# Performance work log

Measured on AMD Instinct MI355X. Metric: run time of the kernel, lower is better.

## Reference

```python
import jax, jax.numpy as jnp
import numpy as np

B, C, H, W = 16, 1, 2048, 128
K8 = 8  # conv1/conv2 expand in_dim -> in_dim*8 channels


def setup_inputs() -> dict:
    key = jax.random.key(0)
    k = jax.random.split(key, 6)
    x = jax.random.normal(k[0], (B, C, H, W), dtype=jnp.float32)
    # 1x1 convs with in_channels=1 reduce to per-output-channel scale + bias
    w1 = jax.random.normal(k[1], (K8,), dtype=jnp.float32) * 0.5
    b1 = jax.random.normal(k[2], (K8,), dtype=jnp.float32) * 0.1
    w2 = jax.random.normal(k[3], (K8,), dtype=jnp.float32) * 0.5
    b2 = jax.random.normal(k[4], (K8,), dtype=jnp.float32) * 0.1
    gamma = jax.random.normal(k[5], (1,), dtype=jnp.float32) * 0.1
    return {"x": x, "w1": w1, "b1": b1, "w2": w2, "b2": b2, "gamma": gamma}


def reference(x, w1, b1, w2, b2, gamma):
    # x: (B,1,H,W)
    # conv1 / conv2: 1x1 conv, 1 -> 8 channels == scale+bias broadcast
    p1 = x * w1[None, :, None, None] + b1[None, :, None, None]  # (B,8,H,W)
    p2 = x * w2[None, :, None, None] + b2[None, :, None, None]  # (B,8,H,W)
    # proj_query: permute(0,2,1,3).reshape(B,H,8W)
    q = p1.transpose(0, 2, 1, 3).reshape(B, H, K8 * W)
    # proj_key: permute(0,1,3,2).reshape(B,8W,H)
    k_ = p2.transpose(0, 1, 3, 2).reshape(B, K8 * W, H)
    energy = jnp.einsum('bhd,bdg->bhg', q, k_)  # (B,H,H)
    mn = energy.min(axis=2, keepdims=True)
    mx = energy.max(axis=2, keepdims=True)
    energy = (energy - mn) / (mx - mn + 1e-8)
    attn = jax.nn.softmax(energy, axis=2)  # (B,H,H)
    # attention.reshape(B,1,H,H) @ x (B,1,H,W) -> (B,1,H,W)
    out = jnp.einsum('bhg,bgw->bhw', attn, x[:, 0])[:, None]
    return gamma * out + x
```

## Files before the change

kernel.cpp:

```cpp
#include <hip/hip_runtime.h>
#include <hip/hip_bf16.h>

#define B_ 16
#define H_ 2048
#define W_ 128

using f32x4  = __attribute__((ext_vector_type(4))) float;
using bf16x8 = __attribute__((ext_vector_type(8))) short;

#define GLOAD_LDS16(g, l) __builtin_amdgcn_global_load_lds( \
    (const __attribute__((address_space(1))) unsigned int*)(g), \
    (__attribute__((address_space(3))) unsigned int*)(l), 16, 0, 0)

__device__ inline short bf16bits(float f) {
    union { __hip_bfloat16 h; short s; } u;
    u.h = __float2bfloat16(f);
    return u.s;
}

__global__ __launch_bounds__(512) void prep(const float* __restrict__ x,
                                            const float* __restrict__ b1,
                                            const float* __restrict__ w2,
                                            short* __restrict__ Xbt,
                                            short* __restrict__ XTt,
                                            float* __restrict__ cs) {
    __shared__ short xs2[8192];
    int b  = blockIdx.x >> 5;
    int g0 = (blockIdx.x & 31) * 64;
    const float* xb = x + ((size_t)b * H_ + g0) * W_;
    short* outb = Xbt + (size_t)b * H_ * W_ + (size_t)g0 * W_;
    short* outt = XTt + (size_t)b * H_ * W_ + (size_t)g0 * W_;
    int t = threadIdx.x;
    float Cc = 0.f;
#pragma unroll
    for (int c = 0; c < 8; ++c) Cc += b1[c] * w2[c];

#pragma unroll
    for (int half = 0; half < 2; ++half) {
        int p = half * 512 + t;
        int row = p >> 4, seg = p & 15;
        const float* src = xb + (size_t)row * W_ + seg * 8;
        float4 v0 = *reinterpret_cast<const float4*>(src);
        float4 v1 = *reinterpret_cast<const float4*>(src + 4);
        bf16x8 v;
        v[0] = bf16bits(v0.x); v[1] = bf16bits(v0.y);
        v[2] = bf16bits(v0.z); v[3] = bf16bits(v0.w);
        v[4] = bf16bits(v1.x); v[5] = bf16bits(v1.y);
        v[6] = bf16bits(v1.z); v[7] = bf16bits(v1.w);
        int chunk = ((row >> 4) * 4 + (seg >> 2)) * 64 + (seg & 3) * 16 + (row & 15);
        *reinterpret_cast<bf16x8*>(outb + (size_t)chunk * 8) = v;
        float s = (v0.x + v0.y + v0.z + v0.w) + (v1.x + v1.y + v1.z + v1.w);
        s += __shfl_xor(s, 1); s += __shfl_xor(s, 2);
        s += __shfl_xor(s, 4); s += __shfl_xor(s, 8);
        if (seg == 0) cs[b * H_ + g0 + row] = Cc * s;
        int c8 = seg ^ ((row >> 3) & 3);
        *reinterpret_cast<bf16x8*>(&xs2[row * 128 + c8 * 8]) = v;
    }
    __syncthreads();
    {
        int r2 = t & 7, qp = (t >> 3) & 3, nt2 = (t >> 5) & 7, kt = t >> 8;
        int w0 = nt2 * 16 + r2 * 2;
        int c8p = (w0 >> 3) ^ qp;
        int gb = kt * 32 + qp * 8;
        bf16x8 lo, hi;
#pragma unroll
        for (int jj = 0; jj < 8; ++jj) {
            unsigned u = *reinterpret_cast<const unsigned*>(
                &xs2[(gb + jj) * 128 + c8p * 8 + (w0 & 7)]);
            lo[jj] = (short)(u & 0xffffu);
            hi[jj] = (short)(u >> 16);
        }
        *reinterpret_cast<bf16x8*>(outt + (size_t)(t * 2) * 8) = lo;
        *reinterpret_cast<bf16x8*>(outt + (size_t)(t * 2 + 1) * 8) = hi;
    }
}

__global__ __launch_bounds__(512, 4) void fused_attn(
    const float* __restrict__ x,
    const short* __restrict__ Xbt, const short* __restrict__ XTt,
    const float* __restrict__ cs,
    const float* __restrict__ w1, const float* __restrict__ w2,
    const float* __restrict__ gamma, float* __restrict__ out) {
    __shared__ __align__(16) char stgA[2][8192];
    __shared__ __align__(16) char stgV[2][8192];
    __shared__ __align__(16) char pb[2][4096];
    __shared__ float red_mn[4][2][16];
    __shared__ float red_mx[4][2][16];
    __shared__ float zred[4][2][16];

    float A = 0.f;
#pragma unroll
    for (int c = 0; c < 8; ++c) A += w1[c] * w2[c];

    int tid = threadIdx.x;
    int wv = tid >> 6, lane = tid & 63;
    int wh = wv >> 1, wg = wv & 1;
    int q = lane >> 4, r = lane & 15;

    int bid = blockIdx.x;
    int swz = (bid & 7) * 64 + (bid >> 3);
    int b = swz >> 5, hb = swz & 31;
    int h_base = hb * 64;

    const char* xbt = (const char*)(Xbt + (size_t)b * H_ * W_);
    const char* xtt = (const char*)(XTt + (size_t)b * H_ * W_);
    const float* csb = cs + b * H_;

    bf16x8 afr[4];
#pragma unroll
    for (int k = 0; k < 4; ++k)
        afr[k] = *reinterpret_cast<const bf16x8*>(
            xbt + ((size_t)(((h_base >> 4) + wh) * 4 + k) * 64 + lane) * 16);

    float mnv = 3.4e38f, mxv = -3.4e38f;
    GLOAD_LDS16(xbt + wv * 1024 + lane * 16, stgA[0] + wv * 1024);
    float4 csv = *reinterpret_cast<const float4*>(csb + wg * 16 + q * 4);
    for (int t = 0; t < 64; ++t) {
        int tn = (t + 1) & 63;
        float4 csn = *reinterpret_cast<const float4*>(csb + tn * 32 + wg * 16 + q * 4);
        GLOAD_LDS16(xbt + (size_t)tn * 8192 + wv * 1024 + lane * 16,
                    stgA[tn & 1] + wv * 1024);
        asm volatile("s_waitcnt vmcnt(2)" ::: "memory");
        __builtin_amdgcn_s_barrier();
        __builtin_amdgcn_sched_barrier(0);
        const char* sa = stgA[t & 1];
        f32x4 s = {0.f, 0.f, 0.f, 0.f};
        __builtin_amdgcn_s_setprio(1);
#pragma unroll
        for (int k = 0; k < 4; ++k) {
            bf16x8 bfr = *reinterpret_cast<const bf16x8*>(sa + ((wg * 4 + k) * 64 + lane) * 16);
            s = __builtin_amdgcn_mfma_f32_16x16x32_bf16(bfr, afr[k], s, 0, 0, 0);
        }
        __builtin_amdgcn_s_setprio(0);
#pragma unroll
        for (int reg = 0; reg < 4; ++reg) {
            float tv = fmaf(A, s[reg], csv[reg]);
            mnv = fminf(mnv, tv); mxv = fmaxf(mxv, tv);
        }
        __builtin_amdgcn_s_barrier();
        __builtin_amdgcn_sched_barrier(0);
        csv = csn;
    }
    mnv = fminf(mnv, __shfl_xor(mnv, 16)); mnv = fminf(mnv, __shfl_xor(mnv, 32));
    mxv = fmaxf(mxv, __shfl_xor(mxv, 16)); mxv = fmaxf(mxv, __shfl_xor(mxv, 32));
    if (lane < 16) { red_mn[wh][wg][lane] = mnv; red_mx[wh][wg][lane] = mxv; }
    __syncthreads();
    const float LOG2E = 1.4426950408889634f;
    float mn = fminf(red_mn[wh][0][r], red_mn[wh][1][r]);
    float mx = fmaxf(red_mx[wh][0][r], red_mx[wh][1][r]);
    float inv = LOG2E / (mx - mn + 1e-8f);
    float c1 = inv, c0v = -mn * inv, A1 = A * inv;

    f32x4 o[4];
#pragma unroll
    for (int i = 0; i < 4; ++i) o[i] = (f32x4){0.f, 0.f, 0.f, 0.f};
    float zacc = 0.f;
    GLOAD_LDS16(xbt + wv * 1024 + lane * 16, stgA[0] + wv * 1024);
    GLOAD_LDS16(xtt + wv * 1024 + lane * 16, stgV[0] + wv * 1024);
    csv = *reinterpret_cast<const float4*>(csb + wg * 16 + q * 4);
    for (int t = 0; t < 64; ++t) {
        int tn = (t + 1) & 63;
        float4 csn = *reinterpret_cast<const float4*>(csb + tn * 32 + wg * 16 + q * 4);
        GLOAD_LDS16(xbt + (size_t)tn * 8192 + wv * 1024 + lane * 16,
                    stgA[tn & 1] + wv * 1024);
        GLOAD_LDS16(xtt + (size_t)tn * 8192 + wv * 1024 + lane * 16,
                    stgV[tn & 1] + wv * 1024);
        asm volatile("s_waitcnt vmcnt(3)" ::: "memory");
        __builtin_amdgcn_s_barrier();
        __builtin_amdgcn_sched_barrier(0);
        const char* sa = stgA[t & 1];
        const char* sv = stgV[t & 1];
        bf16x8 bt[4];
#pragma unroll
        for (int n = 0; n < 4; ++n)
            bt[n] = *reinterpret_cast<const bf16x8*>(sv + ((wg * 4 + n) * 64 + lane) * 16);
        f32x4 s = {0.f, 0.f, 0.f, 0.f};
        __builtin_amdgcn_s_setprio(1);
#pragma unroll
        for (int k = 0; k < 4; ++k) {
            bf16x8 bfr = *reinterpret_cast<const bf16x8*>(sa + ((wg * 4 + k) * 64 + lane) * 16);
            s = __builtin_amdgcn_mfma_f32_16x16x32_bf16(bfr, afr[k], s, 0, 0, 0);
        }
        __builtin_amdgcn_s_setprio(0);
        float e0 = exp2f(fmaf(s[0], A1, fmaf(csv[0], c1, c0v)));
        float e1 = exp2f(fmaf(s[1], A1, fmaf(csv[1], c1, c0v)));
        float e2 = exp2f(fmaf(s[2], A1, fmaf(csv[2], c1, c0v)));
        float e3 = exp2f(fmaf(s[3], A1, fmaf(csv[3], c1, c0v)));
        zacc += (e0 + e1) + (e2 + e3);
        unsigned d0 = (unsigned)(unsigned short)bf16bits(e0) |
                      ((unsigned)(unsigned short)bf16bits(e1) << 16);
        unsigned d1 = (unsigned)(unsigned short)bf16bits(e2) |
                      ((unsigned)(unsigned short)bf16bits(e3) << 16);
        uint2 dd; dd.x = d0; dd.y = d1;
        char* pw = pb[t & 1];
        *reinterpret_cast<uint2*>(
            pw + ((wh * 64 + (wg * 2 + (q >> 1)) * 16 + r) * 16 + (q & 1) * 8)) = dd;
        asm volatile("s_waitcnt lgkmcnt(0)" ::: "memory");
        __builtin_amdgcn_s_barrier();
        __builtin_amdgcn_sched_barrier(0);
        bf16x8 pa = *reinterpret_cast<const bf16x8*>(pw + (wh * 64 + lane) * 16);
        __builtin_amdgcn_s_setprio(1);
#pragma unroll
        for (int n = 0; n < 4; ++n)
            o[n] = __builtin_amdgcn_mfma_f32_16x16x32_bf16(pa, bt[n], o[n], 0, 0, 0);
        __builtin_amdgcn_s_setprio(0);
        csv = csn;
    }

    zacc += __shfl_xor(zacc, 16); zacc += __shfl_xor(zacc, 32);
    if (lane < 16) zred[wh][wg][lane] = zacc;
    __syncthreads();

    float g_ = gamma[0];
#pragma unroll
    for (int reg = 0; reg < 4; ++reg) {
        int hq = q * 4 + reg;
        float z = zred[wh][0][hq] + zred[wh][1][hq];
        float sc = g_ / z;
        int h = h_base + wh * 16 + hq;
#pragma unroll
        for (int n = 0; n < 4; ++n) {
            int w = wg * 64 + n * 16 + r;
            size_t idx = ((size_t)b * H_ + h) * W_ + w;
            out[idx] = fmaf(sc, o[n][reg], x[idx]);
        }
    }
}

extern "C" void kernel_launch(void* const* d_in, const int* in_sizes, int n_in,
                              void* d_out, int out_size, void* d_ws, size_t ws_size,
                              hipStream_t stream) {
    const float* x     = (const float*)d_in[0];
    const float* w1    = (const float*)d_in[1];
    const float* b1    = (const float*)d_in[2];
    const float* w2    = (const float*)d_in[3];
    const float* b2    = (const float*)d_in[4];
    const float* gamma = (const float*)d_in[5];
    float* out = (float*)d_out;
    (void)b2;

    char* ws = (char*)d_ws;
    const size_t XB_BYTES = (size_t)B_ * H_ * W_ * 2;
    short* Xbt = (short*)ws;
    short* XTt = (short*)(ws + XB_BYTES);
    float* cs  = (float*)(ws + 2 * XB_BYTES);

    prep<<<B_ * 32, 512, 0, stream>>>(x, b1, w2, Xbt, XTt, cs);
    fused_attn<<<B_ * H_ / 64, 512, 0, stream>>>(x, Xbt, XTt, cs, w1, w2, gamma, out);
}
```

Before: 163.9 us.

## Keep P in registers via 16x16x16 MFMA, triple-buffer staging, cache cs in LDS

Changes the PV product to the 16x16x16 bf16 MFMA so the softmax probabilities can feed the MFMA directly from registers. This removes the LDS round-trip and the extra barrier on each tile. The V-transpose layout written by prep is changed to match, and each wave-group now splits the H-dimension reduction and accumulates all 128 output columns. The partial results are combined through LDS in the epilogue, which also writes with float4. The staging buffers go from double to triple buffering, with one barrier per iteration, and the per-block cs vector is preloaded into LDS. The cost is higher LDS usage (about 58KB per block, which may reduce occupancy), twice the accumulator registers, and twice as many smaller MFMAs.

After: 152.4 us. 1.08x faster.

```diff
diff --git a/kernel.cpp b/kernel.cpp
--- a/kernel.cpp
+++ b/kernel.cpp
@@ -7,6 +7,7 @@
 
 using f32x4  = __attribute__((ext_vector_type(4))) float;
 using bf16x8 = __attribute__((ext_vector_type(8))) short;
+using bf16x4 = __attribute__((ext_vector_type(4))) short;
 
 #define GLOAD_LDS16(g, l) __builtin_amdgcn_global_load_lds( \
     (const __attribute__((address_space(1))) unsigned int*)(g), \
@@ -22,14 +23,14 @@
                                             const float* __restrict__ b1,
                                             const float* __restrict__ w2,
                                             short* __restrict__ Xbt,
-                                            short* __restrict__ XTt,
+                                            char* __restrict__ XTt,
                                             float* __restrict__ cs) {
     __shared__ short xs2[8192];
     int b  = blockIdx.x >> 5;
     int g0 = (blockIdx.x & 31) * 64;
     const float* xb = x + ((size_t)b * H_ + g0) * W_;
     short* outb = Xbt + (size_t)b * H_ * W_ + (size_t)g0 * W_;
-    short* outt = XTt + (size_t)b * H_ * W_ + (size_t)g0 * W_;
+    char* outt = XTt + (size_t)b * H_ * W_ * 2 + (size_t)g0 * W_ * 2;
     int t = threadIdx.x;
     float Cc = 0.f;
 #pragma unroll
@@ -57,36 +58,42 @@
         *reinterpret_cast<bf16x8*>(&xs2[row * 128 + c8 * 8]) = v;
     }
     __syncthreads();
-    {
-        int r2 = t & 7, qp = (t >> 3) & 3, nt2 = (t >> 5) & 7, kt = t >> 8;
-        int w0 = nt2 * 16 + r2 * 2;
-        int c8p = (w0 >> 3) ^ qp;
-        int gb = kt * 32 + qp * 8;
-        bf16x8 lo, hi;
-#pragma unroll
-        for (int jj = 0; jj < 8; ++jj) {
-            unsigned u = *reinterpret_cast<const unsigned*>(
-                &xs2[(gb + jj) * 128 + c8p * 8 + (w0 & 7)]);
-            lo[jj] = (short)(u & 0xffffu);
-            hi[jj] = (short)(u >> 16);
-        }
-        *reinterpret_cast<bf16x8*>(outt + (size_t)(t * 2) * 8) = lo;
-        *reinterpret_cast<bf16x8*>(outt + (size_t)(t * 2 + 1) * 8) = hi;
+#pragma unroll
+    for (int it2 = 0; it2 < 2; ++it2) {
+        int i = it2 * 512 + t;
+        int rr = i & 7, q = (i >> 3) & 3, n = (i >> 5) & 7, gq = i >> 8;
+        int w0 = n * 16 + rr * 2;
+        int rs = (gq * 2 + (q >> 1)) & 3;
+        int c8p = (w0 >> 3) ^ rs;
+        int gbase = gq * 16 + q * 4;
+        unsigned u0 = *reinterpret_cast<const unsigned*>(&xs2[(gbase + 0) * 128 + c8p * 8 + (w0 & 7)]);
+        unsigned u1 = *reinterpret_cast<const unsigned*>(&xs2[(gbase + 1) * 128 + c8p * 8 + (w0 & 7)]);
+        unsigned u2 = *reinterpret_cast<const unsigned*>(&xs2[(gbase + 2) * 128 + c8p * 8 + (w0 & 7)]);
+        unsigned u3 = *reinterpret_cast<const unsigned*>(&xs2[(gbase + 3) * 128 + c8p * 8 + (w0 & 7)]);
+        uint4 outv;
+        outv.x = (u0 & 0xffffu) | (u1 << 16);
+        outv.y = (u2 & 0xffffu) | (u3 << 16);
+        outv.z = (u0 >> 16) | (u1 & 0xffff0000u);
+        outv.w = (u2 >> 16) | (u3 & 0xffff0000u);
+        int tloc = gq >> 1, gb2 = gq & 1;
+        size_t addr = (size_t)tloc * 8192 + ((gb2 * 8 + n) * 512) + (q * 16 + rr * 2) * 8;
+        *reinterpret_cast<uint4*>(outt + addr) = outv;
     }
 }
 
 __global__ __launch_bounds__(512, 4) void fused_attn(
     const float* __restrict__ x,
-    const short* __restrict__ Xbt, const short* __restrict__ XTt,
+    const short* __restrict__ Xbt, const char* __restrict__ XTt,
     const float* __restrict__ cs,
     const float* __restrict__ w1, const float* __restrict__ w2,
     const float* __restrict__ gamma, float* __restrict__ out) {
-    __shared__ __align__(16) char stgA[2][8192];
-    __shared__ __align__(16) char stgV[2][8192];
-    __shared__ __align__(16) char pb[2][4096];
-    __shared__ float red_mn[4][2][16];
-    __shared__ float red_mx[4][2][16];
-    __shared__ float zred[4][2][16];
+    __shared__ __align__(16) char smem[58880];
+    char* stgA = smem;
+    char* stgV = smem + 24576;
+    float* csl = (float*)(smem + 49152);
+    float* redmn = (float*)(smem + 57344);
+    float* redmx = (float*)(smem + 57856);
+    float* zred  = (float*)(smem + 58368);
 
     float A = 0.f;
 #pragma unroll
@@ -103,7 +110,7 @@
     int h_base = hb * 64;
 
     const char* xbt = (const char*)(Xbt + (size_t)b * H_ * W_);
-    const char* xtt = (const char*)(XTt + (size_t)b * H_ * W_);
+    const char* xtt = XTt + (size_t)b * H_ * W_ * 2;
     const float* csb = cs + b * H_;
 
     bf16x8 afr[4];
@@ -111,19 +118,28 @@
     for (int k = 0; k < 4; ++k)
         afr[k] = *reinterpret_cast<const bf16x8*>(
             xbt + ((size_t)(((h_base >> 4) + wh) * 4 + k) * 64 + lane) * 16);
+    {
+        float4 cv = *reinterpret_cast<const float4*>(csb + tid * 4);
+        *reinterpret_cast<float4*>(csl + tid * 4) = cv;
+    }
+    GLOAD_LDS16(xbt + wv * 1024 + lane * 16, stgA + wv * 1024);
+    __syncthreads();
 
     float mnv = 3.4e38f, mxv = -3.4e38f;
-    GLOAD_LDS16(xbt + wv * 1024 + lane * 16, stgA[0] + wv * 1024);
-    float4 csv = *reinterpret_cast<const float4*>(csb + wg * 16 + q * 4);
+    int cur = 0;
     for (int t = 0; t < 64; ++t) {
-        int tn = (t + 1) & 63;
-        float4 csn = *reinterpret_cast<const float4*>(csb + tn * 32 + wg * 16 + q * 4);
-        GLOAD_LDS16(xbt + (size_t)tn * 8192 + wv * 1024 + lane * 16,
-                    stgA[tn & 1] + wv * 1024);
-        asm volatile("s_waitcnt vmcnt(2)" ::: "memory");
+        int nxt = (cur == 2) ? 0 : cur + 1;
+        if (t < 63) {
+            GLOAD_LDS16(xbt + (size_t)(t + 1) * 8192 + wv * 1024 + lane * 16,
+                        stgA + nxt * 8192 + wv * 1024);
+            asm volatile("s_waitcnt vmcnt(1)" ::: "memory");
+        } else {
+            asm volatile("s_waitcnt vmcnt(0)" ::: "memory");
+        }
         __builtin_amdgcn_s_barrier();
         __builtin_amdgcn_sched_barrier(0);
-        const char* sa = stgA[t & 1];
+        float4 csq = *reinterpret_cast<const float4*>(csl + t * 32 + wg * 16 + q * 4);
+        const char* sa = stgA + cur * 8192;
         f32x4 s = {0.f, 0.f, 0.f, 0.f};
         __builtin_amdgcn_s_setprio(1);
 #pragma unroll
@@ -134,46 +150,47 @@
         __builtin_amdgcn_s_setprio(0);
 #pragma unroll
         for (int reg = 0; reg < 4; ++reg) {
-            float tv = fmaf(A, s[reg], csv[reg]);
+            float tv = fmaf(A, s[reg], csq[reg]);
             mnv = fminf(mnv, tv); mxv = fmaxf(mxv, tv);
+        }
+        cur = nxt;
+    }
+    mnv = fminf(mnv, __shfl_xor(mnv, 16)); mnv = fminf(mnv, __shfl_xor(mnv, 32));
+    mxv = fmaxf(mxv, __shfl_xor(mxv, 16)); mxv = fmaxf(mxv, __shfl_xor(mxv, 32));
+    if (lane < 16) {
+        redmn[(wh * 2 + wg) * 16 + lane] = mnv;
+        redmx[(wh * 2 + wg) * 16 + lane] = mxv;
+    }
+    __syncthreads();
+    const float LOG2E = 1.4426950408889634f;
+    float mn = fminf(redmn[(wh * 2 + 0) * 16 + r], redmn[(wh * 2 + 1) * 16 + r]);
+    float mx = fmaxf(redmx[(wh * 2 + 0) * 16 + r], redmx[(wh * 2 + 1) * 16 + r]);
+    float inv = LOG2E / (mx - mn + 1e-8f);
+    float c1 = inv, c0v = -mn * inv, A1 = A * inv;
+
+    f32x4 o[8];
+#pragma unroll
+    for (int i = 0; i < 8; ++i) o[i] = (f32x4){0.f, 0.f, 0.f, 0.f};
+    float zacc = 0.f;
+    GLOAD_LDS16(xbt + wv * 1024 + lane * 16, stgA + wv * 1024);
+    GLOAD_LDS16(xtt + wv * 1024 + lane * 16, stgV + wv * 1024);
+    cur = 0;
+    for (int t = 0; t < 64; ++t) {
+        int nxt = (cur == 2) ? 0 : cur + 1;
+        if (t < 63) {
+            GLOAD_LDS16(xbt + (size_t)(t + 1) * 8192 + wv * 1024 + lane * 16,
+                        stgA + nxt * 8192 + wv * 1024);
+            GLOAD_LDS16(xtt + (size_t)(t + 1) * 8192 + wv * 1024 + lane * 16,
+                        stgV + nxt * 8192 + wv * 1024);
+            asm volatile("s_waitcnt vmcnt(2)" ::: "memory");
+        } else {
+            asm volatile("s_waitcnt vmcnt(0)" ::: "memory");
         }
         __builtin_amdgcn_s_barrier();
         __builtin_amdgcn_sched_barrier(0);
-        csv = csn;
-    }
-    mnv = fminf(mnv, __shfl_xor(mnv, 16)); mnv = fminf(mnv, __shfl_xor(mnv, 32));
-    mxv = fmaxf(mxv, __shfl_xor(mxv, 16)); mxv = fmaxf(mxv, __shfl_xor(mxv, 32));
-    if (lane < 16) { red_mn[wh][wg][lane] = mnv; red_mx[wh][wg][lane] = mxv; }
-    __syncthreads();
-    const float LOG2E = 1.4426950408889634f;
-    float mn = fminf(red_mn[wh][0][r], red_mn[wh][1][r]);
-    float mx = fmaxf(red_mx[wh][0][r], red_mx[wh][1][r]);
-    float inv = LOG2E / (mx - mn + 1e-8f);
-    float c1 = inv, c0v = -mn * inv, A1 = A * inv;
-
-    f32x4 o[4];
-#pragma unroll
-    for (int i = 0; i < 4; ++i) o[i] = (f32x4){0.f, 0.f, 0.f, 0.f};
-    float zacc = 0.f;
-    GLOAD_LDS16(xbt + wv * 1024 + lane * 16, stgA[0] + wv * 1024);
-    GLOAD_LDS16(xtt + wv * 1024 + lane * 16, stgV[0] + wv * 1024);
-    csv = *reinterpret_cast<const float4*>(csb + wg * 16 + q * 4);
-    for (int t = 0; t < 64; ++t) {
-        int tn = (t + 1) & 63;
-        float4 csn = *reinterpret_cast<const float4*>(csb + tn * 32 + wg * 16 + q * 4);
-        GLOAD_LDS16(xbt + (size_t)tn * 8192 + wv * 1024 + lane * 16,
-                    stgA[tn & 1] + wv * 1024);
-        GLOAD_LDS16(xtt + (size_t)tn * 8192 + wv * 1024 + lane * 16,
-                    stgV[tn & 1] + wv * 1024);
-        asm volatile("s_waitcnt vmcnt(3)" ::: "memory");
-        __builtin_amdgcn_s_barrier();
-        __builtin_amdgcn_sched_barrier(0);
-        const char* sa = stgA[t & 1];
-        const char* sv = stgV[t & 1];
-        bf16x8 bt[4];
-#pragma unroll
-        for (int n = 0; n < 4; ++n)
-            bt[n] = *reinterpret_cast<const bf16x8*>(sv + ((wg * 4 + n) * 64 + lane) * 16);
+        float4 csq = *reinterpret_cast<const float4*>(csl + t * 32 + wg * 16 + q * 4);
+        const char* sa = stgA + cur * 8192;
+        const char* sv = stgV + cur * 8192;
         f32x4 s = {0.f, 0.f, 0.f, 0.f};
         __builtin_amdgcn_s_setprio(1);
 #pragma unroll
@@ -182,47 +199,54 @@
             s = __builtin_amdgcn_mfma_f32_16x16x32_bf16(bfr, afr[k], s, 0, 0, 0);
         }
         __builtin_amdgcn_s_setprio(0);
-        float e0 = exp2f(fmaf(s[0], A1, fmaf(csv[0], c1, c0v)));
-        float e1 = exp2f(fmaf(s[1], A1, fmaf(csv[1], c1, c0v)));
-        float e2 = exp2f(fmaf(s[2], A1, fmaf(csv[2], c1, c0v)));
-        float e3 = exp2f(fmaf(s[3], A1, fmaf(csv[3], c1, c0v)));
+        float e0 = exp2f(fmaf(s[0], A1, fmaf(csq[0], c1, c0v)));
+        float e1 = exp2f(fmaf(s[1], A1, fmaf(csq[1], c1, c0v)));
+        float e2 = exp2f(fmaf(s[2], A1, fmaf(csq[2], c1, c0v)));
+        float e3 = exp2f(fmaf(s[3], A1, fmaf(csq[3], c1, c0v)));
         zacc += (e0 + e1) + (e2 + e3);
-        unsigned d0 = (unsigned)(unsigned short)bf16bits(e0) |
-                      ((unsigned)(unsigned short)bf16bits(e1) << 16);
-        unsigned d1 = (unsigned)(unsigned short)bf16bits(e2) |
-                      ((unsigned)(unsigned short)bf16bits(e3) << 16);
-        uint2 dd; dd.x = d0; dd.y = d1;
-        char* pw = pb[t & 1];
-        *reinterpret_cast<uint2*>(
-            pw + ((wh * 64 + (wg * 2 + (q >> 1)) * 16 + r) * 16 + (q & 1) * 8)) = dd;
-        asm volatile("s_waitcnt lgkmcnt(0)" ::: "memory");
-        __builtin_amdgcn_s_barrier();
-        __builtin_amdgcn_sched_barrier(0);
-        bf16x8 pa = *reinterpret_cast<const bf16x8*>(pw + (wh * 64 + lane) * 16);
+        bf16x4 pf;
+        pf[0] = bf16bits(e0); pf[1] = bf16bits(e1);
+        pf[2] = bf16bits(e2); pf[3] = bf16bits(e3);
         __builtin_amdgcn_s_setprio(1);
 #pragma unroll
-        for (int n = 0; n < 4; ++n)
-            o[n] = __builtin_amdgcn_mfma_f32_16x16x32_bf16(pa, bt[n], o[n], 0, 0, 0);
+        for (int n = 0; n < 8; ++n) {
+            bf16x4 av = *reinterpret_cast<const bf16x4*>(
+                sv + (wg * 8 + n) * 512 + lane * 8);
+            asm("v_mfma_f32_16x16x16_bf16 %0, %1, %2, %0"
+                : "+v"(o[n]) : "v"(av), "v"(pf));
+        }
         __builtin_amdgcn_s_setprio(0);
-        csv = csn;
+        cur = nxt;
     }
 
     zacc += __shfl_xor(zacc, 16); zacc += __shfl_xor(zacc, 32);
-    if (lane < 16) zred[wh][wg][lane] = zacc;
-    __syncthreads();
-
-    float g_ = gamma[0];
-#pragma unroll
-    for (int reg = 0; reg < 4; ++reg) {
-        int hq = q * 4 + reg;
-        float z = zred[wh][0][hq] + zred[wh][1][hq];
-        float sc = g_ / z;
-        int h = h_base + wh * 16 + hq;
-#pragma unroll
-        for (int n = 0; n < 4; ++n) {
-            int w = wg * 64 + n * 16 + r;
-            size_t idx = ((size_t)b * H_ + h) * W_ + w;
-            out[idx] = fmaf(sc, o[n][reg], x[idx]);
+    if (lane < 16) zred[(wh * 2 + wg) * 16 + lane] = zacc;
+    __syncthreads();
+
+    float* ocw = (float*)smem + wh * 2112;
+    if (wg == 0) {
+#pragma unroll
+        for (int n = 0; n < 8; ++n)
+            *reinterpret_cast<float4*>(ocw + r * 132 + n * 16 + q * 4) =
+                (float4){o[n][0], o[n][1], o[n][2], o[n][3]};
+    }
+    __syncthreads();
+    if (wg == 1) {
+        float z = zred[(wh * 2 + 0) * 16 + r] + zred[(wh * 2 + 1) * 16 + r];
+        float sc = gamma[0] / z;
+        int h = h_base + wh * 16 + r;
+        const float* xrow = x + ((size_t)b * H_ + h) * W_;
+        float* orow = out + ((size_t)b * H_ + h) * W_;
+#pragma unroll
+        for (int n = 0; n < 8; ++n) {
+            float4 p0 = *reinterpret_cast<const float4*>(ocw + r * 132 + n * 16 + q * 4);
+            float4 xv = *reinterpret_cast<const float4*>(xrow + n * 16 + q * 4);
+            float4 res;
+            res.x = fmaf(sc, p0.x + o[n][0], xv.x);
+            res.y = fmaf(sc, p0.y + o[n][1], xv.y);
+            res.z = fmaf(sc, p0.z + o[n][2], xv.z);
+            res.w = fmaf(sc, p0.w + o[n][3], xv.w);
+            *reinterpret_cast<float4*>(orow + n * 16 + q * 4) = res;
         }
     }
 }
@@ -242,7 +266,7 @@
     char* ws = (char*)d_ws;
     const size_t XB_BYTES = (size_t)B_ * H_ * W_ * 2;
     short* Xbt = (short*)ws;
-    short* XTt = (short*)(ws + XB_BYTES);
+    char*  XTt = ws + XB_BYTES;
     float* cs  = (float*)(ws + 2 * XB_BYTES);
 
     prep<<<B_ * 32, 512, 0, stream>>>(x, b1, w2, Xbt, XTt, cs);
```
